# Performance work log

Measured on AMD Instinct MI355X. Metric: run time of the kernel, lower is better.

## Reference

```python
import jax, jax.numpy as jnp
import numpy as np

N_NODES = 100000
N_EDGES = 1000000
NODE_DIM = 64
HIDDEN_DIM = 128


def setup_inputs() -> dict:
    key = jax.random.key(0)
    ks = jax.random.split(key, 9)
    x = jax.random.normal(ks[0], (N_NODES, NODE_DIM), dtype=jnp.float32)
    y = jax.random.normal(ks[1], (N_NODES, NODE_DIM), dtype=jnp.float32)
    edge_index = jax.random.randint(ks[2], (2, N_EDGES), 0, N_NODES, dtype=jnp.int64)
    pos_x = jax.random.normal(ks[3], (N_NODES, 3), dtype=jnp.float32)
    pos_y = jax.random.normal(ks[4], (N_NODES, 3), dtype=jnp.float32)
    in_dim = NODE_DIM * 2 + 1
    # Kaiming-uniform-ish init like torch Linear
    lim1 = 1.0 / np.sqrt(in_dim)
    lim2 = 1.0 / np.sqrt(HIDDEN_DIM)
    W1 = jax.random.uniform(ks[5], (in_dim, HIDDEN_DIM), jnp.float32, -lim1, lim1)
    b1 = jax.random.uniform(ks[6], (HIDDEN_DIM,), jnp.float32, -lim1, lim1)
    W2 = jax.random.uniform(ks[7], (HIDDEN_DIM, 1), jnp.float32, -lim2, lim2)
    b2 = jax.random.uniform(ks[8], (1,), jnp.float32, -lim2, lim2)
    return {"x": x, "y": y, "edge_index": edge_index, "pos_x": pos_x,
            "pos_y": pos_y, "W1": W1, "b1": b1, "W2": W2, "b2": b2}


def reference(x, y, edge_index, pos_x, pos_y, W1, b1, W2, b2):
    src = edge_index[0]
    dst = edge_index[1]
    # per-edge euclidean distance between endpoint positions  [E]
    d = pos_x[src] - pos_y[dst]                      # [E, 3]
    dist = jnp.sqrt(jnp.sum(d * d, axis=1))          # [E]
    # gather + concat: [E, node_dim*2 + 1]
    mlp_in = jnp.concatenate([x[src], y[dst], dist[:, None]], axis=1)
    h = jax.nn.relu(mlp_in @ W1 + b1)                # [E, hidden]
    out = jax.nn.relu(h @ W2 + b2)                   # [E, 1]
    return out
```

## Files before the change

kernel.cpp:

```cpp
#include <hip/hip_runtime.h>
#include <hip/hip_bf16.h>


constexpr int NDIM  = 64;
constexpr int HID   = 128;
constexpr int KPAD  = 136;

typedef __attribute__((ext_vector_type(8))) short  short8;
typedef __attribute__((ext_vector_type(4))) int    int4v;
typedef __attribute__((ext_vector_type(4))) float  floatx4;

__device__ __forceinline__ short f2bf(float f) {
    union { __hip_bfloat16 h; short s; } cv;
    cv.h = __float2bfloat16(f);
    return cv.s;
}

__device__ __forceinline__ int pack2(float a, float b) {
    union { __hip_bfloat162 h; int u; } cv;
    cv.h = __float22bfloat162_rn(float2{a, b});
    return cv.u;
}

__device__ __forceinline__ short8 make_afrag_f32(const float* rp) {
    const floatx4 f0 = *reinterpret_cast<const floatx4*>(rp);
    const floatx4 f1 = *reinterpret_cast<const floatx4*>(rp + 4);
    union { int4v i; short8 s8; } cv;
    cv.i.x = pack2(f0.x, f0.y);
    cv.i.y = pack2(f0.z, f0.w);
    cv.i.z = pack2(f1.x, f1.y);
    cv.i.w = pack2(f1.z, f1.w);
    return cv.s8;
}

__global__ __launch_bounds__(256) void cvt_kernel(
    const float* __restrict__ xin, const float* __restrict__ yin,
    short* __restrict__ xb, short* __restrict__ yb, int nfl)
{
    const int stride = gridDim.x * blockDim.x;
    const int n8 = nfl >> 3;
    for (int i = blockIdx.x * blockDim.x + threadIdx.x; i < n8; i += stride) {
        {
            const floatx4 f0 = *reinterpret_cast<const floatx4*>(xin + i * 8);
            const floatx4 f1 = *reinterpret_cast<const floatx4*>(xin + i * 8 + 4);
            union { int4v v; short8 s; } c;
            c.v.x = pack2(f0.x, f0.y); c.v.y = pack2(f0.z, f0.w);
            c.v.z = pack2(f1.x, f1.y); c.v.w = pack2(f1.z, f1.w);
            *reinterpret_cast<short8*>(xb + i * 8) = c.s;
        }
        {
            const floatx4 f0 = *reinterpret_cast<const floatx4*>(yin + i * 8);
            const floatx4 f1 = *reinterpret_cast<const floatx4*>(yin + i * 8 + 4);
            union { int4v v; short8 s; } c;
            c.v.x = pack2(f0.x, f0.y); c.v.y = pack2(f0.z, f0.w);
            c.v.z = pack2(f1.x, f1.y); c.v.w = pack2(f1.z, f1.w);
            *reinterpret_cast<short8*>(yb + i * 8) = c.s;
        }
    }
}

template <bool BF16GATHER>
__global__ __launch_bounds__(256, 3) void edge_mlp_kernel(
    const float* __restrict__ x, const float* __restrict__ y,
    const short* __restrict__ xb, const short* __restrict__ yb,
    const int*  __restrict__ ei, const float* __restrict__ px,
    const float* __restrict__ py, const float* __restrict__ W1,
    const float* __restrict__ b1, const float* __restrict__ W2,
    const float* __restrict__ b2, float* __restrict__ out, int E)
{
    __shared__ __align__(16) short Wt[HID * KPAD];

    const int tid = threadIdx.x;

    for (int base = 0; base < HID * HID; base += 256 * 8) {
        float f[8];
#pragma unroll
        for (int u = 0; u < 8; ++u) f[u] = W1[base + u * 256 + tid];
#pragma unroll
        for (int u = 0; u < 8; ++u) {
            int i = base + u * 256 + tid;
            Wt[(i & 127) * KPAD + (i >> 7)] = f2bf(f[u]);
        }
    }
    if (tid < HID) {
        const int n = tid;
        Wt[n * KPAD + 128] = f2bf(W1[128 * HID + n]);
        Wt[n * KPAD + 129] = f2bf(b1[n]);
#pragma unroll
        for (int j = 130; j < 136; ++j) Wt[n * KPAD + j] = 0;
    }
    __syncthreads();

    const int lane = tid & 63;
    const int wave = tid >> 6;
    const int quad = lane >> 4;
    const int lm   = lane & 15;

    float w2v[8];
#pragma unroll
    for (int t = 0; t < 8; ++t) w2v[t] = W2[t * 16 + lm];
    const float b2s = b2[0];

    const int* __restrict__ srcp = ei;
    const int* __restrict__ dstp = ei + E;

    const int sel5 = (quad == 0) ? 128 : 0;

    const int ntiles = (E + 127) / 128;
    for (int tile = blockIdx.x; tile < ntiles; tile += gridDim.x) {
        const int mb = tile * 128 + wave * 32;
        int m0 = mb + lm;       if (m0 >= E) m0 = E - 1;
        int m1 = mb + 16 + lm;  if (m1 >= E) m1 = E - 1;
        const int src0 = srcp[m0], dst0 = dstp[m0];
        const int src1 = srcp[m1], dst1 = dstp[m1];

        const float dx0 = px[src0 * 3 + 0] - py[dst0 * 3 + 0];
        const float dy0 = px[src0 * 3 + 1] - py[dst0 * 3 + 1];
        const float dz0 = px[src0 * 3 + 2] - py[dst0 * 3 + 2];
        const float dist0 = sqrtf(dx0 * dx0 + dy0 * dy0 + dz0 * dz0);
        const float dx1 = px[src1 * 3 + 0] - py[dst1 * 3 + 0];
        const float dy1 = px[src1 * 3 + 1] - py[dst1 * 3 + 1];
        const float dz1 = px[src1 * 3 + 2] - py[dst1 * 3 + 2];
        const float dist1 = sqrtf(dx1 * dx1 + dy1 * dy1 + dz1 * dz1);

        short8 fa[4], fb[4];
#pragma unroll
        for (int s = 0; s < 4; ++s) {
            const int kk = s * 32 + quad * 8;
            if (BF16GATHER) {
                const short* pa = (s < 2) ? (xb + src0 * NDIM + kk)
                                          : (yb + dst0 * NDIM + (kk - 64));
                const short* pb = (s < 2) ? (xb + src1 * NDIM + kk)
                                          : (yb + dst1 * NDIM + (kk - 64));
                fa[s] = *reinterpret_cast<const short8*>(pa);
                fb[s] = *reinterpret_cast<const short8*>(pb);
            } else {
                fa[s] = make_afrag_f32((s < 2) ? (x + src0 * NDIM + kk)
                                               : (y + dst0 * NDIM + (kk - 64)));
                fb[s] = make_afrag_f32((s < 2) ? (x + src1 * NDIM + kk)
                                               : (y + dst1 * NDIM + (kk - 64)));
            }
        }
        short8 fa4, fb4;
        {
            union { int4v i; short8 s8; } ca, cb;
            const int d0 = (quad == 0) ? pack2(dist0, 1.0f) : 0;
            const int d1 = (quad == 0) ? pack2(dist1, 1.0f) : 0;
            ca.i = int4v{d0, 0, 0, 0};
            cb.i = int4v{d1, 0, 0, 0};
            fa4 = ca.s8; fb4 = cb.s8;
        }

        floatx4 accA[8], accB[8];
#pragma unroll
        for (int t = 0; t < 8; ++t) {
            accA[t] = floatx4{0.f, 0.f, 0.f, 0.f};
            accB[t] = floatx4{0.f, 0.f, 0.f, 0.f};
        }

        int zoff = 0;
        asm volatile("" : "+v"(zoff));
        const short* wr  = Wt + zoff + lm * KPAD + quad * 8;
        const short* wr5 = Wt + zoff + lm * KPAD + sel5;

#pragma unroll
        for (int t = 0; t < 8; ++t) {
            const short* base = wr + t * (16 * KPAD);
            const short8 bg0 = *reinterpret_cast<const short8*>(base);
            const short8 bg1 = *reinterpret_cast<const short8*>(base + 32);
            const short8 bg2 = *reinterpret_cast<const short8*>(base + 64);
            const short8 bg3 = *reinterpret_cast<const short8*>(base + 96);
            const short8 bg4 = *reinterpret_cast<const short8*>(wr5 + t * (16 * KPAD));
            accA[t] = __builtin_amdgcn_mfma_f32_16x16x32_bf16(fa[0], bg0, accA[t], 0, 0, 0);
            accB[t] = __builtin_amdgcn_mfma_f32_16x16x32_bf16(fb[0], bg0, accB[t], 0, 0, 0);
            accA[t] = __builtin_amdgcn_mfma_f32_16x16x32_bf16(fa[1], bg1, accA[t], 0, 0, 0);
            accB[t] = __builtin_amdgcn_mfma_f32_16x16x32_bf16(fb[1], bg1, accB[t], 0, 0, 0);
            accA[t] = __builtin_amdgcn_mfma_f32_16x16x32_bf16(fa[2], bg2, accA[t], 0, 0, 0);
            accB[t] = __builtin_amdgcn_mfma_f32_16x16x32_bf16(fb[2], bg2, accB[t], 0, 0, 0);
            accA[t] = __builtin_amdgcn_mfma_f32_16x16x32_bf16(fa[3], bg3, accA[t], 0, 0, 0);
            accB[t] = __builtin_amdgcn_mfma_f32_16x16x32_bf16(fb[3], bg3, accB[t], 0, 0, 0);
            accA[t] = __builtin_amdgcn_mfma_f32_16x16x32_bf16(fa4,  bg4, accA[t], 0, 0, 0);
            accB[t] = __builtin_amdgcn_mfma_f32_16x16x32_bf16(fb4,  bg4, accB[t], 0, 0, 0);
        }

        float p0 = 0.f, p1 = 0.f, p2 = 0.f, p3 = 0.f;
        float q0 = 0.f, q1 = 0.f, q2 = 0.f, q3 = 0.f;
#pragma unroll
        for (int t = 0; t < 8; ++t) {
            p0 += fmaxf(accA[t][0], 0.f) * w2v[t];
            p1 += fmaxf(accA[t][1], 0.f) * w2v[t];
            p2 += fmaxf(accA[t][2], 0.f) * w2v[t];
            p3 += fmaxf(accA[t][3], 0.f) * w2v[t];
            q0 += fmaxf(accB[t][0], 0.f) * w2v[t];
            q1 += fmaxf(accB[t][1], 0.f) * w2v[t];
            q2 += fmaxf(accB[t][2], 0.f) * w2v[t];
            q3 += fmaxf(accB[t][3], 0.f) * w2v[t];
        }
#pragma unroll
        for (int off = 1; off < 16; off <<= 1) {
            p0 += __shfl_xor(p0, off, 64);
            p1 += __shfl_xor(p1, off, 64);
            p2 += __shfl_xor(p2, off, 64);
            p3 += __shfl_xor(p3, off, 64);
            q0 += __shfl_xor(q0, off, 64);
            q1 += __shfl_xor(q1, off, 64);
            q2 += __shfl_xor(q2, off, 64);
            q3 += __shfl_xor(q3, off, 64);
        }
        if (lm < 4) {
            const float vA = (lm == 0) ? p0 : (lm == 1) ? p1 : (lm == 2) ? p2 : p3;
            const float vB = (lm == 0) ? q0 : (lm == 1) ? q1 : (lm == 2) ? q2 : q3;
            const int eA = mb + quad * 4 + lm;
            const int eB = mb + 16 + quad * 4 + lm;
            if (eA < E) out[eA] = fmaxf(vA + b2s, 0.f);
            if (eB < E) out[eB] = fmaxf(vB + b2s, 0.f);
        }
    }
}

extern "C" void kernel_launch(void* const* d_in, const int* in_sizes, int n_in,
                              void* d_out, int out_size, void* d_ws, size_t ws_size,
                              hipStream_t stream)
{
    const float* x  = (const float*)d_in[0];
    const float* y  = (const float*)d_in[1];
    const int*   ei = (const int*)  d_in[2];
    const float* px = (const float*)d_in[3];
    const float* py = (const float*)d_in[4];
    const float* W1 = (const float*)d_in[5];
    const float* b1 = (const float*)d_in[6];
    const float* W2 = (const float*)d_in[7];
    const float* b2 = (const float*)d_in[8];
    float* out = (float*)d_out;
    const int E = in_sizes[2] / 2;
    const int nnode_elems = in_sizes[0];

    const size_t need = (size_t)nnode_elems * 2 * sizeof(short);
    if (ws_size >= need) {
        short* xb = (short*)d_ws;
        short* yb = xb + nnode_elems;
        cvt_kernel<<<dim3(1024), dim3(256), 0, stream>>>(x, y, xb, yb, nnode_elems);
        edge_mlp_kernel<true><<<dim3(768), dim3(256), 0, stream>>>(
            x, y, xb, yb, ei, px, py, W1, b1, W2, b2, out, E);
    } else {
        edge_mlp_kernel<false><<<dim3(768), dim3(256), 0, stream>>>(
            x, y, nullptr, nullptr, ei, px, py, W1, b1, W2, b2, out, E);
    }
}
```

Measured before the change: 163.6 us.

## Software-pipeline edge gathers across tiles with double-buffered index/feature registers

Restructures the persistent tile loop into a two-stage software pipeline. Indices are prefetched two tiles ahead and features and positions one tile ahead, so gather latency overlaps the MFMA compute of the current tile. The compute also folds the ReLU/W2 reduction into each hidden-column step, so it no longer holds all 16 accumulators at once and frees registers. The cost is higher register pressure from the duplicate fragment buffers, which could lower occupancy under launch_bounds(256,3).

```diff
diff --git a/kernel.cpp b/kernel.cpp
--- a/kernel.cpp
+++ b/kernel.cpp
@@ -59,6 +59,133 @@
     }
 }
 
+struct IdxB  { int s0, d0, s1, d1; };
+struct PosB  { float ax0, ay0, az0, bx0, by0, bz0;
+               float ax1, ay1, az1, bx1, by1, bz1; };
+struct FragB { short8 fa[4]; short8 fb[4]; };
+
+__device__ __forceinline__ void load_idx(int tile, int wave, int lm, int E,
+    const int* __restrict__ srcp, const int* __restrict__ dstp, IdxB& I)
+{
+    const int mb = tile * 128 + wave * 32;
+    int m0 = mb + lm;       if (m0 >= E) m0 = E - 1;
+    int m1 = mb + 16 + lm;  if (m1 >= E) m1 = E - 1;
+    I.s0 = srcp[m0]; I.d0 = dstp[m0];
+    I.s1 = srcp[m1]; I.d1 = dstp[m1];
+}
+
+__device__ __forceinline__ void load_pos(const IdxB& I,
+    const float* __restrict__ px, const float* __restrict__ py, PosB& P)
+{
+    P.ax0 = px[I.s0 * 3 + 0]; P.ay0 = px[I.s0 * 3 + 1]; P.az0 = px[I.s0 * 3 + 2];
+    P.bx0 = py[I.d0 * 3 + 0]; P.by0 = py[I.d0 * 3 + 1]; P.bz0 = py[I.d0 * 3 + 2];
+    P.ax1 = px[I.s1 * 3 + 0]; P.ay1 = px[I.s1 * 3 + 1]; P.az1 = px[I.s1 * 3 + 2];
+    P.bx1 = py[I.d1 * 3 + 0]; P.by1 = py[I.d1 * 3 + 1]; P.bz1 = py[I.d1 * 3 + 2];
+}
+
+template <bool BF16GATHER>
+__device__ __forceinline__ void load_frags(const IdxB& I,
+    const float* __restrict__ x, const float* __restrict__ y,
+    const short* __restrict__ xb, const short* __restrict__ yb,
+    int quad, FragB& F)
+{
+#pragma unroll
+    for (int s = 0; s < 4; ++s) {
+        const int kk = s * 32 + quad * 8;
+        if (BF16GATHER) {
+            const short* pa = (s < 2) ? (xb + I.s0 * NDIM + kk)
+                                      : (yb + I.d0 * NDIM + (kk - 64));
+            const short* pb = (s < 2) ? (xb + I.s1 * NDIM + kk)
+                                      : (yb + I.d1 * NDIM + (kk - 64));
+            F.fa[s] = *reinterpret_cast<const short8*>(pa);
+            F.fb[s] = *reinterpret_cast<const short8*>(pb);
+        } else {
+            F.fa[s] = make_afrag_f32((s < 2) ? (x + I.s0 * NDIM + kk)
+                                             : (y + I.d0 * NDIM + (kk - 64)));
+            F.fb[s] = make_afrag_f32((s < 2) ? (x + I.s1 * NDIM + kk)
+                                             : (y + I.d1 * NDIM + (kk - 64)));
+        }
+    }
+}
+
+__device__ __forceinline__ void compute_tile(const PosB& P, const FragB& F,
+    int tile, int E, const short* Wt, int lm, int quad, int wave, int sel5,
+    const float* w2v, float b2s, float* __restrict__ out)
+{
+    const float dx0 = P.ax0 - P.bx0, dy0 = P.ay0 - P.by0, dz0 = P.az0 - P.bz0;
+    const float dist0 = sqrtf(dx0 * dx0 + dy0 * dy0 + dz0 * dz0);
+    const float dx1 = P.ax1 - P.bx1, dy1 = P.ay1 - P.by1, dz1 = P.az1 - P.bz1;
+    const float dist1 = sqrtf(dx1 * dx1 + dy1 * dy1 + dz1 * dz1);
+
+    short8 fa4, fb4;
+    {
+        union { int4v i; short8 s8; } ca, cb;
+        const int d0 = (quad == 0) ? pack2(dist0, 1.0f) : 0;
+        const int d1 = (quad == 0) ? pack2(dist1, 1.0f) : 0;
+        ca.i = int4v{d0, 0, 0, 0};
+        cb.i = int4v{d1, 0, 0, 0};
+        fa4 = ca.s8; fb4 = cb.s8;
+    }
+
+    float p0 = 0.f, p1 = 0.f, p2 = 0.f, p3 = 0.f;
+    float q0 = 0.f, q1 = 0.f, q2 = 0.f, q3 = 0.f;
+
+    int zoff = 0;
+    asm volatile("" : "+v"(zoff));
+    const short* wr  = Wt + zoff + lm * KPAD + quad * 8;
+    const short* wr5 = Wt + zoff + lm * KPAD + sel5;
+
+#pragma unroll
+    for (int t = 0; t < 8; ++t) {
+        const short* base = wr + t * (16 * KPAD);
+        const short8 bg0 = *reinterpret_cast<const short8*>(base);
+        const short8 bg1 = *reinterpret_cast<const short8*>(base + 32);
+        const short8 bg2 = *reinterpret_cast<const short8*>(base + 64);
+        const short8 bg3 = *reinterpret_cast<const short8*>(base + 96);
+        const short8 bg4 = *reinterpret_cast<const short8*>(wr5 + t * (16 * KPAD));
+        floatx4 A{0.f, 0.f, 0.f, 0.f}, B{0.f, 0.f, 0.f, 0.f};
+        A = __builtin_amdgcn_mfma_f32_16x16x32_bf16(F.fa[0], bg0, A, 0, 0, 0);
+        B = __builtin_amdgcn_mfma_f32_16x16x32_bf16(F.fb[0], bg0, B, 0, 0, 0);
+        A = __builtin_amdgcn_mfma_f32_16x16x32_bf16(F.fa[1], bg1, A, 0, 0, 0);
+        B = __builtin_amdgcn_mfma_f32_16x16x32_bf16(F.fb[1], bg1, B, 0, 0, 0);
+        A = __builtin_amdgcn_mfma_f32_16x16x32_bf16(F.fa[2], bg2, A, 0, 0, 0);
+        B = __builtin_amdgcn_mfma_f32_16x16x32_bf16(F.fb[2], bg2, B, 0, 0, 0);
+        A = __builtin_amdgcn_mfma_f32_16x16x32_bf16(F.fa[3], bg3, A, 0, 0, 0);
+        B = __builtin_amdgcn_mfma_f32_16x16x32_bf16(F.fb[3], bg3, B, 0, 0, 0);
+        A = __builtin_amdgcn_mfma_f32_16x16x32_bf16(fa4,    bg4, A, 0, 0, 0);
+        B = __builtin_amdgcn_mfma_f32_16x16x32_bf16(fb4,    bg4, B, 0, 0, 0);
+        p0 += fmaxf(A[0], 0.f) * w2v[t];
+        p1 += fmaxf(A[1], 0.f) * w2v[t];
+        p2 += fmaxf(A[2], 0.f) * w2v[t];
+        p3 += fmaxf(A[3], 0.f) * w2v[t];
+        q0 += fmaxf(B[0], 0.f) * w2v[t];
+        q1 += fmaxf(B[1], 0.f) * w2v[t];
+        q2 += fmaxf(B[2], 0.f) * w2v[t];
+        q3 += fmaxf(B[3], 0.f) * w2v[t];
+    }
+
+#pragma unroll
+    for (int off = 1; off < 16; off <<= 1) {
+        p0 += __shfl_xor(p0, off, 64);
+        p1 += __shfl_xor(p1, off, 64);
+        p2 += __shfl_xor(p2, off, 64);
+        p3 += __shfl_xor(p3, off, 64);
+        q0 += __shfl_xor(q0, off, 64);
+        q1 += __shfl_xor(q1, off, 64);
+        q2 += __shfl_xor(q2, off, 64);
+        q3 += __shfl_xor(q3, off, 64);
+    }
+    if (lm < 4) {
+        const int mb = tile * 128 + wave * 32;
+        const float vA = (lm == 0) ? p0 : (lm == 1) ? p1 : (lm == 2) ? p2 : p3;
+        const float vB = (lm == 0) ? q0 : (lm == 1) ? q1 : (lm == 2) ? q2 : q3;
+        const int eA = mb + quad * 4 + lm;
+        const int eB = mb + 16 + quad * 4 + lm;
+        if (eA < E) out[eA] = fmaxf(vA + b2s, 0.f);
+        if (eB < E) out[eB] = fmaxf(vB + b2s, 0.f);
+    }
+}
+
 template <bool BF16GATHER>
 __global__ __launch_bounds__(256, 3) void edge_mlp_kernel(
     const float* __restrict__ x, const float* __restrict__ y,
@@ -107,114 +234,31 @@
     const int sel5 = (quad == 0) ? 128 : 0;
 
     const int ntiles = (E + 127) / 128;
-    for (int tile = blockIdx.x; tile < ntiles; tile += gridDim.x) {
-        const int mb = tile * 128 + wave * 32;
-        int m0 = mb + lm;       if (m0 >= E) m0 = E - 1;
-        int m1 = mb + 16 + lm;  if (m1 >= E) m1 = E - 1;
-        const int src0 = srcp[m0], dst0 = dstp[m0];
-        const int src1 = srcp[m1], dst1 = dstp[m1];
-
-        const float dx0 = px[src0 * 3 + 0] - py[dst0 * 3 + 0];
-        const float dy0 = px[src0 * 3 + 1] - py[dst0 * 3 + 1];
-        const float dz0 = px[src0 * 3 + 2] - py[dst0 * 3 + 2];
-        const float dist0 = sqrtf(dx0 * dx0 + dy0 * dy0 + dz0 * dz0);
-        const float dx1 = px[src1 * 3 + 0] - py[dst1 * 3 + 0];
-        const float dy1 = px[src1 * 3 + 1] - py[dst1 * 3 + 1];
-        const float dz1 = px[src1 * 3 + 2] - py[dst1 * 3 + 2];
-        const float dist1 = sqrtf(dx1 * dx1 + dy1 * dy1 + dz1 * dz1);
-
-        short8 fa[4], fb[4];
-#pragma unroll
-        for (int s = 0; s < 4; ++s) {
-            const int kk = s * 32 + quad * 8;
-            if (BF16GATHER) {
-                const short* pa = (s < 2) ? (xb + src0 * NDIM + kk)
-                                          : (yb + dst0 * NDIM + (kk - 64));
-                const short* pb = (s < 2) ? (xb + src1 * NDIM + kk)
-                                          : (yb + dst1 * NDIM + (kk - 64));
-                fa[s] = *reinterpret_cast<const short8*>(pa);
-                fb[s] = *reinterpret_cast<const short8*>(pb);
-            } else {
-                fa[s] = make_afrag_f32((s < 2) ? (x + src0 * NDIM + kk)
-                                               : (y + dst0 * NDIM + (kk - 64)));
-                fb[s] = make_afrag_f32((s < 2) ? (x + src1 * NDIM + kk)
-                                               : (y + dst1 * NDIM + (kk - 64)));
-            }
-        }
-        short8 fa4, fb4;
-        {
-            union { int4v i; short8 s8; } ca, cb;
-            const int d0 = (quad == 0) ? pack2(dist0, 1.0f) : 0;
-            const int d1 = (quad == 0) ? pack2(dist1, 1.0f) : 0;
-            ca.i = int4v{d0, 0, 0, 0};
-            cb.i = int4v{d1, 0, 0, 0};
-            fa4 = ca.s8; fb4 = cb.s8;
-        }
-
-        floatx4 accA[8], accB[8];
-#pragma unroll
-        for (int t = 0; t < 8; ++t) {
-            accA[t] = floatx4{0.f, 0.f, 0.f, 0.f};
-            accB[t] = floatx4{0.f, 0.f, 0.f, 0.f};
-        }
-
-        int zoff = 0;
-        asm volatile("" : "+v"(zoff));
-        const short* wr  = Wt + zoff + lm * KPAD + quad * 8;
-        const short* wr5 = Wt + zoff + lm * KPAD + sel5;
-
-#pragma unroll
-        for (int t = 0; t < 8; ++t) {
-            const short* base = wr + t * (16 * KPAD);
-            const short8 bg0 = *reinterpret_cast<const short8*>(base);
-            const short8 bg1 = *reinterpret_cast<const short8*>(base + 32);
-            const short8 bg2 = *reinterpret_cast<const short8*>(base + 64);
-            const short8 bg3 = *reinterpret_cast<const short8*>(base + 96);
-            const short8 bg4 = *reinterpret_cast<const short8*>(wr5 + t * (16 * KPAD));
-            accA[t] = __builtin_amdgcn_mfma_f32_16x16x32_bf16(fa[0], bg0, accA[t], 0, 0, 0);
-            accB[t] = __builtin_amdgcn_mfma_f32_16x16x32_bf16(fb[0], bg0, accB[t], 0, 0, 0);
-            accA[t] = __builtin_amdgcn_mfma_f32_16x16x32_bf16(fa[1], bg1, accA[t], 0, 0, 0);
-            accB[t] = __builtin_amdgcn_mfma_f32_16x16x32_bf16(fb[1], bg1, accB[t], 0, 0, 0);
-            accA[t] = __builtin_amdgcn_mfma_f32_16x16x32_bf16(fa[2], bg2, accA[t], 0, 0, 0);
-            accB[t] = __builtin_amdgcn_mfma_f32_16x16x32_bf16(fb[2], bg2, accB[t], 0, 0, 0);
-            accA[t] = __builtin_amdgcn_mfma_f32_16x16x32_bf16(fa[3], bg3, accA[t], 0, 0, 0);
-            accB[t] = __builtin_amdgcn_mfma_f32_16x16x32_bf16(fb[3], bg3, accB[t], 0, 0, 0);
-            accA[t] = __builtin_amdgcn_mfma_f32_16x16x32_bf16(fa4,  bg4, accA[t], 0, 0, 0);
-            accB[t] = __builtin_amdgcn_mfma_f32_16x16x32_bf16(fb4,  bg4, accB[t], 0, 0, 0);
-        }
-
-        float p0 = 0.f, p1 = 0.f, p2 = 0.f, p3 = 0.f;
-        float q0 = 0.f, q1 = 0.f, q2 = 0.f, q3 = 0.f;
-#pragma unroll
-        for (int t = 0; t < 8; ++t) {
-            p0 += fmaxf(accA[t][0], 0.f) * w2v[t];
-            p1 += fmaxf(accA[t][1], 0.f) * w2v[t];
-            p2 += fmaxf(accA[t][2], 0.f) * w2v[t];
-            p3 += fmaxf(accA[t][3], 0.f) * w2v[t];
-            q0 += fmaxf(accB[t][0], 0.f) * w2v[t];
-            q1 += fmaxf(accB[t][1], 0.f) * w2v[t];
-            q2 += fmaxf(accB[t][2], 0.f) * w2v[t];
-            q3 += fmaxf(accB[t][3], 0.f) * w2v[t];
-        }
-#pragma unroll
-        for (int off = 1; off < 16; off <<= 1) {
-            p0 += __shfl_xor(p0, off, 64);
-            p1 += __shfl_xor(p1, off, 64);
-            p2 += __shfl_xor(p2, off, 64);
-            p3 += __shfl_xor(p3, off, 64);
-            q0 += __shfl_xor(q0, off, 64);
-            q1 += __shfl_xor(q1, off, 64);
-            q2 += __shfl_xor(q2, off, 64);
-            q3 += __shfl_xor(q3, off, 64);
-        }
-        if (lm < 4) {
-            const float vA = (lm == 0) ? p0 : (lm == 1) ? p1 : (lm == 2) ? p2 : p3;
-            const float vB = (lm == 0) ? q0 : (lm == 1) ? q1 : (lm == 2) ? q2 : q3;
-            const int eA = mb + quad * 4 + lm;
-            const int eB = mb + 16 + quad * 4 + lm;
-            if (eA < E) out[eA] = fmaxf(vA + b2s, 0.f);
-            if (eB < E) out[eB] = fmaxf(vB + b2s, 0.f);
-        }
+    const int step = gridDim.x;
+    int tile = blockIdx.x;
+    if (tile >= ntiles) return;
+
+    IdxB Ia, Ib; PosB Pa, Pb; FragB Fa, Fb;
+    load_idx(tile,        wave, lm, E, srcp, dstp, Ia);
+    load_idx(tile + step, wave, lm, E, srcp, dstp, Ib);
+    load_pos(Ia, px, py, Pa);
+    load_frags<BF16GATHER>(Ia, x, y, xb, yb, quad, Fa);
+
+#pragma unroll 1
+    for (;;) {
+        load_frags<BF16GATHER>(Ib, x, y, xb, yb, quad, Fb);
+        load_pos(Ib, px, py, Pb);
+        load_idx(tile + 2 * step, wave, lm, E, srcp, dstp, Ia);
+        compute_tile(Pa, Fa, tile, E, Wt, lm, quad, wave, sel5, w2v, b2s, out);
+        tile += step;
+        if (tile >= ntiles) break;
+
+        load_frags<BF16GATHER>(Ia, x, y, xb, yb, quad, Fa);
+        load_pos(Ia, px, py, Pa);
+        load_idx(tile + 2 * step, wave, lm, E, srcp, dstp, Ib);
+        compute_tile(Pb, Fb, tile, E, Wt, lm, quad, wave, sel5, w2v, b2s, out);
+        tile += step;
+        if (tile >= ntiles) break;
     }
 }
 
```

Result: no change. 166.0 us (+1.5%).

## Cut register pressure to raise occupancy to four blocks per CU

Applied to the files above, without the earlier changes.

The hidden-layer MFMA loop now runs in two halves of four output tiles, with a scheduling barrier between them. Each half is reduced into the second-layer partial sums right away, so only half the accumulators are live at once. The per-edge distance is computed once per edge by 32 lanes and broadcast with shuffles, instead of every lane doing redundant position gathers. With fewer registers in use, launch bounds go to four blocks per CU and the grid to 1024 blocks, aiming for more latency hiding on the gathers; the risk is a less overlapped MFMA schedule across the barrier.

```diff
diff --git a/kernel.cpp b/kernel.cpp
--- a/kernel.cpp
+++ b/kernel.cpp
@@ -60,7 +60,7 @@
 }
 
 template <bool BF16GATHER>
-__global__ __launch_bounds__(256, 3) void edge_mlp_kernel(
+__global__ __launch_bounds__(256, 4) void edge_mlp_kernel(
     const float* __restrict__ x, const float* __restrict__ y,
     const short* __restrict__ xb, const short* __restrict__ yb,
     const int*  __restrict__ ei, const float* __restrict__ px,
@@ -114,14 +114,17 @@
         const int src0 = srcp[m0], dst0 = dstp[m0];
         const int src1 = srcp[m1], dst1 = dstp[m1];
 
-        const float dx0 = px[src0 * 3 + 0] - py[dst0 * 3 + 0];
-        const float dy0 = px[src0 * 3 + 1] - py[dst0 * 3 + 1];
-        const float dz0 = px[src0 * 3 + 2] - py[dst0 * 3 + 2];
-        const float dist0 = sqrtf(dx0 * dx0 + dy0 * dy0 + dz0 * dz0);
-        const float dx1 = px[src1 * 3 + 0] - py[dst1 * 3 + 0];
-        const float dy1 = px[src1 * 3 + 1] - py[dst1 * 3 + 1];
-        const float dz1 = px[src1 * 3 + 2] - py[dst1 * 3 + 2];
-        const float dist1 = sqrtf(dx1 * dx1 + dy1 * dy1 + dz1 * dz1);
+        float dd = 0.f;
+        if (lane < 32) {
+            const int ps = (lane < 16) ? src0 : src1;
+            const int pd = (lane < 16) ? dst0 : dst1;
+            const float ax = px[ps * 3 + 0] - py[pd * 3 + 0];
+            const float ay = px[ps * 3 + 1] - py[pd * 3 + 1];
+            const float az = px[ps * 3 + 2] - py[pd * 3 + 2];
+            dd = sqrtf(ax * ax + ay * ay + az * az);
+        }
+        const float dist0 = __shfl(dd, lm, 64);
+        const float dist1 = __shfl(dd, lm + 16, 64);
 
         short8 fa[4], fb[4];
 #pragma unroll
@@ -151,12 +154,8 @@
             fa4 = ca.s8; fb4 = cb.s8;
         }
 
-        floatx4 accA[8], accB[8];
-#pragma unroll
-        for (int t = 0; t < 8; ++t) {
-            accA[t] = floatx4{0.f, 0.f, 0.f, 0.f};
-            accB[t] = floatx4{0.f, 0.f, 0.f, 0.f};
-        }
+        float p0 = 0.f, p1 = 0.f, p2 = 0.f, p3 = 0.f;
+        float q0 = 0.f, q1 = 0.f, q2 = 0.f, q3 = 0.f;
 
         int zoff = 0;
         asm volatile("" : "+v"(zoff));
@@ -164,38 +163,49 @@
         const short* wr5 = Wt + zoff + lm * KPAD + sel5;
 
 #pragma unroll
-        for (int t = 0; t < 8; ++t) {
-            const short* base = wr + t * (16 * KPAD);
-            const short8 bg0 = *reinterpret_cast<const short8*>(base);
-            const short8 bg1 = *reinterpret_cast<const short8*>(base + 32);
-            const short8 bg2 = *reinterpret_cast<const short8*>(base + 64);
-            const short8 bg3 = *reinterpret_cast<const short8*>(base + 96);
-            const short8 bg4 = *reinterpret_cast<const short8*>(wr5 + t * (16 * KPAD));
-            accA[t] = __builtin_amdgcn_mfma_f32_16x16x32_bf16(fa[0], bg0, accA[t], 0, 0, 0);
-            accB[t] = __builtin_amdgcn_mfma_f32_16x16x32_bf16(fb[0], bg0, accB[t], 0, 0, 0);
-            accA[t] = __builtin_amdgcn_mfma_f32_16x16x32_bf16(fa[1], bg1, accA[t], 0, 0, 0);
-            accB[t] = __builtin_amdgcn_mfma_f32_16x16x32_bf16(fb[1], bg1, accB[t], 0, 0, 0);
-            accA[t] = __builtin_amdgcn_mfma_f32_16x16x32_bf16(fa[2], bg2, accA[t], 0, 0, 0);
-            accB[t] = __builtin_amdgcn_mfma_f32_16x16x32_bf16(fb[2], bg2, accB[t], 0, 0, 0);
-            accA[t] = __builtin_amdgcn_mfma_f32_16x16x32_bf16(fa[3], bg3, accA[t], 0, 0, 0);
-            accB[t] = __builtin_amdgcn_mfma_f32_16x16x32_bf16(fb[3], bg3, accB[t], 0, 0, 0);
-            accA[t] = __builtin_amdgcn_mfma_f32_16x16x32_bf16(fa4,  bg4, accA[t], 0, 0, 0);
-            accB[t] = __builtin_amdgcn_mfma_f32_16x16x32_bf16(fb4,  bg4, accB[t], 0, 0, 0);
-        }
-
-        float p0 = 0.f, p1 = 0.f, p2 = 0.f, p3 = 0.f;
-        float q0 = 0.f, q1 = 0.f, q2 = 0.f, q3 = 0.f;
-#pragma unroll
-        for (int t = 0; t < 8; ++t) {
-            p0 += fmaxf(accA[t][0], 0.f) * w2v[t];
-            p1 += fmaxf(accA[t][1], 0.f) * w2v[t];
-            p2 += fmaxf(accA[t][2], 0.f) * w2v[t];
-            p3 += fmaxf(accA[t][3], 0.f) * w2v[t];
-            q0 += fmaxf(accB[t][0], 0.f) * w2v[t];
-            q1 += fmaxf(accB[t][1], 0.f) * w2v[t];
-            q2 += fmaxf(accB[t][2], 0.f) * w2v[t];
-            q3 += fmaxf(accB[t][3], 0.f) * w2v[t];
-        }
+        for (int half = 0; half < 2; ++half) {
+            if (half) __builtin_amdgcn_sched_barrier(0);
+
+            floatx4 aA[4], aB[4];
+#pragma unroll
+            for (int u = 0; u < 4; ++u) {
+                aA[u] = floatx4{0.f, 0.f, 0.f, 0.f};
+                aB[u] = floatx4{0.f, 0.f, 0.f, 0.f};
+            }
+#pragma unroll
+            for (int u = 0; u < 4; ++u) {
+                const int t = half * 4 + u;
+                const short* base = wr + t * (16 * KPAD);
+                const short8 bg0 = *reinterpret_cast<const short8*>(base);
+                const short8 bg1 = *reinterpret_cast<const short8*>(base + 32);
+                const short8 bg2 = *reinterpret_cast<const short8*>(base + 64);
+                const short8 bg3 = *reinterpret_cast<const short8*>(base + 96);
+                const short8 bg4 = *reinterpret_cast<const short8*>(wr5 + t * (16 * KPAD));
+                aA[u] = __builtin_amdgcn_mfma_f32_16x16x32_bf16(fa[0], bg0, aA[u], 0, 0, 0);
+                aB[u] = __builtin_amdgcn_mfma_f32_16x16x32_bf16(fb[0], bg0, aB[u], 0, 0, 0);
+                aA[u] = __builtin_amdgcn_mfma_f32_16x16x32_bf16(fa[1], bg1, aA[u], 0, 0, 0);
+                aB[u] = __builtin_amdgcn_mfma_f32_16x16x32_bf16(fb[1], bg1, aB[u], 0, 0, 0);
+                aA[u] = __builtin_amdgcn_mfma_f32_16x16x32_bf16(fa[2], bg2, aA[u], 0, 0, 0);
+                aB[u] = __builtin_amdgcn_mfma_f32_16x16x32_bf16(fb[2], bg2, aB[u], 0, 0, 0);
+                aA[u] = __builtin_amdgcn_mfma_f32_16x16x32_bf16(fa[3], bg3, aA[u], 0, 0, 0);
+                aB[u] = __builtin_amdgcn_mfma_f32_16x16x32_bf16(fb[3], bg3, aB[u], 0, 0, 0);
+                aA[u] = __builtin_amdgcn_mfma_f32_16x16x32_bf16(fa4,   bg4, aA[u], 0, 0, 0);
+                aB[u] = __builtin_amdgcn_mfma_f32_16x16x32_bf16(fb4,   bg4, aB[u], 0, 0, 0);
+            }
+#pragma unroll
+            for (int u = 0; u < 4; ++u) {
+                const float w = w2v[half * 4 + u];
+                p0 += fmaxf(aA[u][0], 0.f) * w;
+                p1 += fmaxf(aA[u][1], 0.f) * w;
+                p2 += fmaxf(aA[u][2], 0.f) * w;
+                p3 += fmaxf(aA[u][3], 0.f) * w;
+                q0 += fmaxf(aB[u][0], 0.f) * w;
+                q1 += fmaxf(aB[u][1], 0.f) * w;
+                q2 += fmaxf(aB[u][2], 0.f) * w;
+                q3 += fmaxf(aB[u][3], 0.f) * w;
+            }
+        }
+
 #pragma unroll
         for (int off = 1; off < 16; off <<= 1) {
             p0 += __shfl_xor(p0, off, 64);
@@ -240,10 +250,10 @@
         short* xb = (short*)d_ws;
         short* yb = xb + nnode_elems;
         cvt_kernel<<<dim3(1024), dim3(256), 0, stream>>>(x, y, xb, yb, nnode_elems);
-        edge_mlp_kernel<true><<<dim3(768), dim3(256), 0, stream>>>(
+        edge_mlp_kernel<true><<<dim3(1024), dim3(256), 0, stream>>>(
             x, y, xb, yb, ei, px, py, W1, b1, W2, b2, out, E);
     } else {
-        edge_mlp_kernel<false><<<dim3(768), dim3(256), 0, stream>>>(
+        edge_mlp_kernel<false><<<dim3(1024), dim3(256), 0, stream>>>(
             x, y, nullptr, nullptr, ei, px, py, W1, b1, W2, b2, out, E);
     }
 }
```

After: 163.3 us, median of 2. About the same (-0.2%).
